# Performance work log

Hardware: AMD Instinct MI355X
Metric: run time of the kernel (lower is better)

## Reference

```python
import jax, jax.numpy as jnp
import numpy as np
import math

B, S, D = 2, 2048, 512
H = 8
DK = D // H  # 64


def setup_inputs() -> dict:
    key = jax.random.key(0)
    ks = jax.random.split(key, 9)
    inp = {
        "query": jax.random.normal(ks[0], (B, S, D), jnp.float32),
        "key": jax.random.normal(ks[1], (B, S, D), jnp.float32),
        "value": jax.random.normal(ks[2], (B, S, D), jnp.float32),
        "attn_weight": jax.random.normal(ks[3], (B, H, S, S), jnp.float32),
        "mask": jax.random.randint(ks[4], (B, S), 0, 2).astype(bool),
        # nn.Linear(d_model, d_model, bias=False) weights, applied as x @ W.T
        "Wq": jax.random.normal(ks[5], (D, D), jnp.float32) / math.sqrt(D),
        "Wk": jax.random.normal(ks[6], (D, D), jnp.float32) / math.sqrt(D),
        "Wv": jax.random.normal(ks[7], (D, D), jnp.float32) / math.sqrt(D),
        "Wo": jax.random.normal(ks[8], (D, D), jnp.float32) / math.sqrt(D),
    }
    return inp


def reference(query, key, value, attn_weight, mask, Wq, Wk, Wv, Wo):
    b, s, d = query.shape
    # project and split heads: [b, h, s, dk]
    def split_heads(x, W):
        return (x @ W.T).reshape(b, -1, H, DK).transpose(0, 2, 1, 3)

    q = split_heads(query, Wq)
    k = split_heads(key, Wk)
    v = split_heads(value, Wv)

    scores = jnp.einsum("bhqd,bhkd->bhqk", q, k) / math.sqrt(DK)
    # mask broadcast as [b,1,1,s]: True -> -inf over keys (applied before bias subtraction,
    # matching torch order; -inf - finite stays -inf)
    scores = jnp.where(mask[:, None, None, :], -jnp.inf, scores)
    scores = scores - attn_weight
    p_attn = jax.nn.softmax(scores, axis=-1)  # dropout p=0 (eval) -> identity
    x = jnp.einsum("bhqk,bhkd->bhqd", p_attn, v)
    x = x.transpose(0, 2, 1, 3).reshape(b, -1, H * DK)
    return x @ Wo.T
```

## Files before the change

### kernel.cpp

```cpp
#include <hip/hip_runtime.h>
#include <math.h>

typedef __bf16 bf16;
typedef __bf16 bf16x8 __attribute__((ext_vector_type(8)));
typedef float f32x4 __attribute__((ext_vector_type(4)));
typedef unsigned int u32;
typedef unsigned long long u64;

#define MFMA_BF16(a, b, c) __builtin_amdgcn_mfma_f32_16x16x32_bf16((a), (b), (c), 0, 0, 0)

static constexpr int kB = 2;
static constexpr int kS = 2048;
static constexpr int kD = 512;
static constexpr int kH = 8;
static constexpr int kDK = 64;
static constexpr int kTileBytes = 8192;
static constexpr int kBhBytes = 32 * kTileBytes;

__global__ void detect_mask_kernel(const unsigned char* __restrict__ m,
                                   u32* __restrict__ bm) {
  __shared__ int sh;
  const int tid = threadIdx.x;
  if (tid == 0) sh = 0;
  __syncthreads();
  int any = 0;
  for (int i = tid; i < kB * kS; i += 256)
    if ((i & 3) != 0 && m[i] != 0) any = 1;
  if (any) atomicOr(&sh, 1);
  __syncthreads();
  const bool as_bool = (sh != 0);
  for (int wi = tid; wi < kB * kS / 32; wi += 256) {
    u32 word = 0;
    const int base = wi * 32;
    for (int j = 0; j < 32; j++) {
      const bool mv = as_bool ? (m[base + j] != 0) : (((const int*)m)[base + j] != 0);
      word |= (mv ? 1u : 0u) << j;
    }
    bm[wi] = word;
  }
}

__device__ __forceinline__ void cvt16(const float* __restrict__ p, bf16x8& v0, bf16x8& v1) {
  const float4 fA = ((const float4*)p)[0];
  const float4 fB = ((const float4*)p)[1];
  const float4 fC = ((const float4*)p)[2];
  const float4 fD = ((const float4*)p)[3];
  v0[0] = (bf16)fA.x; v0[1] = (bf16)fA.y; v0[2] = (bf16)fA.z; v0[3] = (bf16)fA.w;
  v0[4] = (bf16)fB.x; v0[5] = (bf16)fB.y; v0[6] = (bf16)fB.z; v0[7] = (bf16)fB.w;
  v1[0] = (bf16)fC.x; v1[1] = (bf16)fC.y; v1[2] = (bf16)fC.z; v1[3] = (bf16)fC.w;
  v1[4] = (bf16)fD.x; v1[5] = (bf16)fD.y; v1[6] = (bf16)fD.z; v1[7] = (bf16)fD.w;
}

template <bool A_IS_F32, int MODE>
__device__ __forceinline__ void gemm_body(const void* __restrict__ Aptr,
                                          const float* __restrict__ Wptr,
                                          void* __restrict__ dst) {
  constexpr bool TRANS = (MODE != 2);
  __shared__ bf16 As[128][40];
  __shared__ bf16 Bs[128][40];

  const int tid = threadIdx.x;
  const int lane = tid & 63;
  const int w = tid >> 6;
  const int wr = w >> 1, wc = w & 1;
  const int l16 = lane & 15, g = lane >> 4;

  const int m_tile = blockIdx.x * 128;
  const int n_tile = blockIdx.y * 128;

  f32x4 acc[4][4] = {};

  const int sr = tid >> 1;
  const int sc = (tid & 1) * 16;

  for (int k0 = 0; k0 < kD; k0 += 32) {
    if constexpr (A_IS_F32) {
      const float* ap = (const float*)Aptr + (size_t)(m_tile + sr) * kD + k0 + sc;
      bf16x8 v0, v1;
      cvt16(ap, v0, v1);
      *(bf16x8*)&As[sr][sc] = v0;
      *(bf16x8*)&As[sr][sc + 8] = v1;
    } else {
      const bf16* ap = (const bf16*)Aptr + (size_t)(m_tile + sr) * kD + k0 + sc;
      *(bf16x8*)&As[sr][sc] = *(const bf16x8*)ap;
      *(bf16x8*)&As[sr][sc + 8] = *(const bf16x8*)(ap + 8);
    }
    {
      const float* bp = Wptr + (size_t)(n_tile + sr) * kD + k0 + sc;
      bf16x8 v0, v1;
      cvt16(bp, v0, v1);
      *(bf16x8*)&Bs[sr][sc] = v0;
      *(bf16x8*)&Bs[sr][sc + 8] = v1;
    }
    __syncthreads();

    bf16x8 a[4], bfr[4];
    #pragma unroll
    for (int i = 0; i < 4; i++)
      a[i] = *(const bf16x8*)&As[wr * 64 + i * 16 + l16][g * 8];
    #pragma unroll
    for (int i = 0; i < 4; i++)
      bfr[i] = *(const bf16x8*)&Bs[wc * 64 + i * 16 + l16][g * 8];
    #pragma unroll
    for (int mi = 0; mi < 4; mi++)
      #pragma unroll
      for (int ni = 0; ni < 4; ni++) {
        if constexpr (TRANS)
          acc[mi][ni] = MFMA_BF16(bfr[ni], a[mi], acc[mi][ni]);
        else
          acc[mi][ni] = MFMA_BF16(a[mi], bfr[ni], acc[mi][ni]);
      }
    __syncthreads();
  }

  #pragma unroll
  for (int mi = 0; mi < 4; mi++) {
    #pragma unroll
    for (int ni = 0; ni < 4; ni++) {
      const f32x4 v = acc[mi][ni];
      if constexpr (TRANS) {
        const int gm = m_tile + wr * 64 + mi * 16 + l16;
        const int gn0 = n_tile + wc * 64 + ni * 16 + g * 4;
        if constexpr (MODE == 3) {
          *(float4*)&((float*)dst)[(size_t)gm * kD + gn0] =
              (float4){v[0], v[1], v[2], v[3]};
        } else {
          const int bi = gm >> 11;
          const int s = gm & (kS - 1);
          const int h = gn0 >> 6;
          const int dk0 = gn0 & (kDK - 1);
          union { bf16 hh[4]; u64 u; } pk;
          pk.hh[0] = (bf16)v[0]; pk.hh[1] = (bf16)v[1];
          pk.hh[2] = (bf16)v[2]; pk.hh[3] = (bf16)v[3];
          if constexpr (MODE == 0) {
            *(u64*)&((bf16*)dst)[(((size_t)bi * kH + h) * kS + s) * kDK + dk0] = pk.u;
          } else {
            char* base = (char*)dst + (size_t)(bi * kH + h) * kBhBytes + (s >> 6) * kTileBytes;
            *(u64*)(base + (s & 63) * 128 + ((dk0 * 2) ^ ((s & 7) << 4))) = pk.u;
          }
        }
      } else {
        const int gm0 = m_tile + wr * 64 + mi * 16 + g * 4;
        const int gn = n_tile + wc * 64 + ni * 16 + l16;
        const int bi = gm0 >> 11;
        const int s0 = gm0 & (kS - 1);
        const int h = gn >> 6;
        const int dk = gn & (kDK - 1);
        union { bf16 hh[4]; u64 u; } pk;
        pk.hh[0] = (bf16)v[0]; pk.hh[1] = (bf16)v[1];
        pk.hh[2] = (bf16)v[2]; pk.hh[3] = (bf16)v[3];
        char* base = (char*)dst + (size_t)(bi * kH + h) * kBhBytes + (s0 >> 6) * kTileBytes;
        *(u64*)(base + dk * 128 + (((s0 & 63) * 2) ^ ((dk & 7) << 4))) = pk.u;
      }
    }
  }
}

__global__ __launch_bounds__(256) void proj_kernel(
    const float* __restrict__ q, const float* __restrict__ k, const float* __restrict__ v,
    const float* __restrict__ Wq, const float* __restrict__ Wk, const float* __restrict__ Wv,
    bf16* __restrict__ qw, bf16* __restrict__ kw, bf16* __restrict__ vtw) {
  const int z = blockIdx.z;
  if (z == 0) gemm_body<true, 0>(q, Wq, qw);
  else if (z == 1) gemm_body<true, 1>(k, Wk, kw);
  else gemm_body<true, 2>(v, Wv, vtw);
}

__global__ __launch_bounds__(256) void out_kernel(const bf16* __restrict__ x,
                                                  const float* __restrict__ Wo,
                                                  float* __restrict__ out) {
  gemm_body<false, 3>(x, Wo, out);
}

__global__ __launch_bounds__(256, 2) void attn_kernel(
    const bf16* __restrict__ qw, const char* __restrict__ kw,
    const char* __restrict__ vt, const float* __restrict__ bias,
    const u32* __restrict__ bmask, bf16* __restrict__ xw) {
  __shared__ char KV[2][2][kTileBytes];
  __shared__ u32 Ps[4][16][36];
  __shared__ u32 mask_lds[64];

  const int tid = threadIdx.x;
  const int lane = tid & 63;
  const int w = tid >> 6;
  const int l16 = lane & 15, g = lane >> 4;

  const int bid = blockIdx.x;
  const int xcd = bid & 7;
  const int j = bid >> 3;
  const int bh = xcd * 2 + (j >> 5);
  const int qb = j & 31;
  const int b = bh >> 3;
  const int hh = bh & 7;
  const int qr0 = qb * 64 + w * 16;

  if (tid < 64) mask_lds[tid] = bmask[b * 64 + tid];
  __syncthreads();

  const bf16* qrow = qw + ((size_t)bh * kS + qr0 + l16) * kDK;
  const bf16x8 aq0 = *(const bf16x8*)(qrow + g * 8);
  const bf16x8 aq1 = *(const bf16x8*)(qrow + 32 + g * 8);

  const float* brow = bias + ((size_t)bh * kS + qr0 + l16) * kS;
  const char* ktile = kw + (size_t)bh * kBhBytes;
  const char* vtile = vt + (size_t)bh * kBhBytes;

  f32x4 o[4] = {};
  float m_run = -__builtin_inff();
  float l_run = 0.f;
  const int swz = (l16 & 7) << 4;

  auto dma_tile = [&](int tile, int nb) {
    const char* kg = ktile + (size_t)tile * kTileBytes + w * 2048 + lane * 16;
    __builtin_amdgcn_global_load_lds(
        (const __attribute__((address_space(1))) void*)kg,
        (__attribute__((address_space(3))) void*)&KV[nb][0][w * 2048], 16, 0, 0);
    __builtin_amdgcn_global_load_lds(
        (const __attribute__((address_space(1))) void*)(kg + 1024),
        (__attribute__((address_space(3))) void*)&KV[nb][0][w * 2048 + 1024], 16, 0, 0);
    const char* vg = vtile + (size_t)tile * kTileBytes + w * 2048 + lane * 16;
    __builtin_amdgcn_global_load_lds(
        (const __attribute__((address_space(1))) void*)vg,
        (__attribute__((address_space(3))) void*)&KV[nb][1][w * 2048], 16, 0, 0);
    __builtin_amdgcn_global_load_lds(
        (const __attribute__((address_space(1))) void*)(vg + 1024),
        (__attribute__((address_space(3))) void*)&KV[nb][1][w * 2048 + 1024], 16, 0, 0);
  };
  auto load_bias_asm = [&](f32x4 (&bv)[4], int tile) {
    const float* p0 = brow + tile * 64 + g * 4;
    asm volatile("global_load_dwordx4 %0, %1, off" : "=v"(bv[0]) : "v"(p0));
    asm volatile("global_load_dwordx4 %0, %1, off" : "=v"(bv[1]) : "v"(p0 + 16));
    asm volatile("global_load_dwordx4 %0, %1, off" : "=v"(bv[2]) : "v"(p0 + 32));
    asm volatile("global_load_dwordx4 %0, %1, off" : "=v"(bv[3]) : "v"(p0 + 48));
  };

  auto phase = [&](int t, f32x4 (&bc)[4], f32x4 (&bn)[4]) {
    const int cur = t & 1, nxt = cur ^ 1;
    const int tp = (t + 1) & 31;
    dma_tile(tp, nxt);
    load_bias_asm(bn, tp);

    const char* kb0 = &KV[cur][0][0];
    const char* vb0 = &KV[cur][1][0];
    bf16x8 kf[4][2];
    #pragma unroll
    for (int nf = 0; nf < 4; nf++) {
      const int r = nf * 16 + l16;
      #pragma unroll
      for (int h = 0; h < 2; h++)
        kf[nf][h] = *(const bf16x8*)(kb0 + r * 128 + ((g * 16 + h * 64) ^ swz));
    }
    bf16x8 vf[2][4];
    #pragma unroll
    for (int kb2 = 0; kb2 < 2; kb2++)
      #pragma unroll
      for (int ni = 0; ni < 4; ni++) {
        const int d = ni * 16 + l16;
        vf[kb2][ni] = *(const bf16x8*)(vb0 + d * 128 + ((kb2 * 64 + g * 16) ^ swz));
      }

    const u32 w0 = mask_lds[2 * t];
    const u32 w1 = mask_lds[2 * t + 1];

    f32x4 sf[4];
    __builtin_amdgcn_s_setprio(1);
    #pragma unroll
    for (int nf = 0; nf < 4; nf++) {
      f32x4 z = {};
      z = MFMA_BF16(kf[nf][0], aq0, z);
      z = MFMA_BF16(kf[nf][1], aq1, z);
      sf[nf] = z;
    }
    __builtin_amdgcn_s_setprio(0);

    asm volatile("s_waitcnt vmcnt(8)" ::: "memory");
    __builtin_amdgcn_sched_barrier(0);

    float p[4][4];
    float tmax = -__builtin_inff();
    #pragma unroll
    for (int nf = 0; nf < 4; nf++) {
      const u32 wsel = (nf < 2) ? w0 : w1;
      #pragma unroll
      for (int r = 0; r < 4; r++) {
        float sv = sf[nf][r] * 0.125f - bc[nf][r];
        const int bp = (nf & 1) * 16 + g * 4 + r;
        if ((wsel >> bp) & 1) sv = -__builtin_inff();
        p[nf][r] = sv;
        tmax = fmaxf(tmax, sv);
      }
    }
    tmax = fmaxf(tmax, __shfl_xor(tmax, 16, 64));
    tmax = fmaxf(tmax, __shfl_xor(tmax, 32, 64));

    const float mnew = fmaxf(m_run, tmax);
    const float scale = (m_run == -__builtin_inff()) ? 0.f : __expf(m_run - mnew);
    const float mexp = (mnew == -__builtin_inff()) ? 0.f : mnew;
    float psum = 0.f;
    #pragma unroll
    for (int nf = 0; nf < 4; nf++)
      #pragma unroll
      for (int r = 0; r < 4; r++) {
        const float pv = __expf(p[nf][r] - mexp);
        p[nf][r] = pv;
        psum += pv;
      }
    psum += __shfl_xor(psum, 16, 64);
    psum += __shfl_xor(psum, 32, 64);
    m_run = mnew;
    l_run = l_run * scale + psum;
    #pragma unroll
    for (int ni = 0; ni < 4; ni++) o[ni] *= scale;

    #pragma unroll
    for (int nf = 0; nf < 4; nf++) {
      union { bf16 h[2]; u32 u; } c0, c1;
      c0.h[0] = (bf16)p[nf][0]; c0.h[1] = (bf16)p[nf][1];
      c1.h[0] = (bf16)p[nf][2]; c1.h[1] = (bf16)p[nf][3];
      Ps[w][l16][nf * 8 + g * 2] = c0.u;
      Ps[w][l16][nf * 8 + g * 2 + 1] = c1.u;
    }
    asm volatile("s_waitcnt lgkmcnt(0)" ::: "memory");

    __builtin_amdgcn_s_setprio(1);
    #pragma unroll
    for (int kb2 = 0; kb2 < 2; kb2++) {
      const bf16x8 pb = *(const bf16x8*)&Ps[w][l16][kb2 * 16 + g * 4];
      #pragma unroll
      for (int ni = 0; ni < 4; ni++)
        o[ni] = MFMA_BF16(vf[kb2][ni], pb, o[ni]);
    }
    __builtin_amdgcn_s_setprio(0);

    asm volatile("s_waitcnt vmcnt(4)" ::: "memory");
    __builtin_amdgcn_s_barrier();
    __builtin_amdgcn_sched_barrier(0);
  };

  f32x4 bc[4], bn[4];
  dma_tile(0, 0);
  load_bias_asm(bc, 0);
  asm volatile("s_waitcnt vmcnt(4)" ::: "memory");
  __builtin_amdgcn_s_barrier();
  __builtin_amdgcn_sched_barrier(0);

  for (int t = 0; t < 32; t += 2) {
    phase(t, bc, bn);
    phase(t + 1, bn, bc);
  }

  const float inv = (l_run > 0.f) ? 1.f / l_run : 0.f;
  bf16* dstp = xw + ((size_t)b * kS + qr0 + l16) * kD + hh * kDK;
  #pragma unroll
  for (int ni = 0; ni < 4; ni++) {
    union { bf16 h[2]; u32 u; } c0, c1;
    c0.h[0] = (bf16)(o[ni][0] * inv); c0.h[1] = (bf16)(o[ni][1] * inv);
    c1.h[0] = (bf16)(o[ni][2] * inv); c1.h[1] = (bf16)(o[ni][3] * inv);
    *(u32*)&dstp[ni * 16 + g * 4] = c0.u;
    *(u32*)&dstp[ni * 16 + g * 4 + 2] = c1.u;
  }
}

extern "C" void kernel_launch(void* const* d_in, const int* in_sizes, int n_in,
                              void* d_out, int out_size, void* d_ws, size_t ws_size,
                              hipStream_t stream) {
  (void)in_sizes; (void)n_in; (void)out_size; (void)ws_size;
  const float* query = (const float*)d_in[0];
  const float* key_in = (const float*)d_in[1];
  const float* value = (const float*)d_in[2];
  const float* attnw = (const float*)d_in[3];
  const unsigned char* mask = (const unsigned char*)d_in[4];
  const float* Wq = (const float*)d_in[5];
  const float* Wk = (const float*)d_in[6];
  const float* Wv = (const float*)d_in[7];
  const float* Wo = (const float*)d_in[8];

  const size_t nqkv = (size_t)kB * kH * kS * kDK;
  size_t off = 0;
  auto alloc = [&](size_t bytes) {
    void* p = (char*)d_ws + off;
    off = (off + bytes + 255) & ~(size_t)255;
    return p;
  };
  u32* bm = (u32*)alloc(kB * kS / 32 * 4);
  bf16* q_ws = (bf16*)alloc(nqkv * 2);
  char* k_ws = (char*)alloc(nqkv * 2);
  char* vt_ws = (char*)alloc(nqkv * 2);
  bf16* x_ws = (bf16*)alloc((size_t)kB * kS * kD * 2);

  detect_mask_kernel<<<1, 256, 0, stream>>>(mask, bm);

  proj_kernel<<<dim3(32, 4, 3), dim3(256), 0, stream>>>(query, key_in, value, Wq, Wk, Wv,
                                                        q_ws, (bf16*)k_ws, (bf16*)vt_ws);
  attn_kernel<<<dim3(512), dim3(256), 0, stream>>>(q_ws, k_ws, vt_ws, attnw, bm, x_ws);
  out_kernel<<<dim3(32, 4), dim3(256), 0, stream>>>(x_ws, Wo, (float*)d_out);
}
```

Baseline: 141.7 us.

## Triple-buffer attention K/V tiles with two-ahead prefetch and widen GEMM K-step

The attention kernel moves from double to triple buffering of K/V tiles in LDS. It prefetches K/V and bias two tiles ahead and rotates four bias register sets, with the vmcnt waits retuned to match. This gives more time to hide global load latency, at the cost of more LDS, more registers and redundant reloads of the last tile. Separately, the projection and output GEMMs now step K by 64 instead of 32, which halves the number of barrier-separated iterations and doubles the MFMAs issued per LDS fill.

Result: slower. 168.1 us (+18.7%).

```diff
diff --git a/kernel.cpp b/kernel.cpp
--- a/kernel.cpp
+++ b/kernel.cpp
@@ -56,8 +56,8 @@
                                           const float* __restrict__ Wptr,
                                           void* __restrict__ dst) {
   constexpr bool TRANS = (MODE != 2);
-  __shared__ bf16 As[128][40];
-  __shared__ bf16 Bs[128][40];
+  __shared__ bf16 As[128][72];
+  __shared__ bf16 Bs[128][72];
 
   const int tid = threadIdx.x;
   const int lane = tid & 63;
@@ -71,44 +71,56 @@
   f32x4 acc[4][4] = {};
 
   const int sr = tid >> 1;
-  const int sc = (tid & 1) * 16;
-
-  for (int k0 = 0; k0 < kD; k0 += 32) {
+  const int sc = (tid & 1) * 32;
+
+  for (int k0 = 0; k0 < kD; k0 += 64) {
     if constexpr (A_IS_F32) {
       const float* ap = (const float*)Aptr + (size_t)(m_tile + sr) * kD + k0 + sc;
-      bf16x8 v0, v1;
+      bf16x8 v0, v1, v2, v3;
       cvt16(ap, v0, v1);
+      cvt16(ap + 16, v2, v3);
       *(bf16x8*)&As[sr][sc] = v0;
       *(bf16x8*)&As[sr][sc + 8] = v1;
+      *(bf16x8*)&As[sr][sc + 16] = v2;
+      *(bf16x8*)&As[sr][sc + 24] = v3;
     } else {
       const bf16* ap = (const bf16*)Aptr + (size_t)(m_tile + sr) * kD + k0 + sc;
       *(bf16x8*)&As[sr][sc] = *(const bf16x8*)ap;
       *(bf16x8*)&As[sr][sc + 8] = *(const bf16x8*)(ap + 8);
+      *(bf16x8*)&As[sr][sc + 16] = *(const bf16x8*)(ap + 16);
+      *(bf16x8*)&As[sr][sc + 24] = *(const bf16x8*)(ap + 24);
     }
     {
       const float* bp = Wptr + (size_t)(n_tile + sr) * kD + k0 + sc;
-      bf16x8 v0, v1;
+      bf16x8 v0, v1, v2, v3;
       cvt16(bp, v0, v1);
+      cvt16(bp + 16, v2, v3);
       *(bf16x8*)&Bs[sr][sc] = v0;
       *(bf16x8*)&Bs[sr][sc + 8] = v1;
+      *(bf16x8*)&Bs[sr][sc + 16] = v2;
+      *(bf16x8*)&Bs[sr][sc + 24] = v3;
     }
     __syncthreads();
 
-    bf16x8 a[4], bfr[4];
+    bf16x8 a[4][2], bfr[4][2];
     #pragma unroll
     for (int i = 0; i < 4; i++)
-      a[i] = *(const bf16x8*)&As[wr * 64 + i * 16 + l16][g * 8];
-    #pragma unroll
-    for (int i = 0; i < 4; i++)
-      bfr[i] = *(const bf16x8*)&Bs[wc * 64 + i * 16 + l16][g * 8];
+      #pragma unroll
+      for (int h = 0; h < 2; h++) {
+        a[i][h] = *(const bf16x8*)&As[wr * 64 + i * 16 + l16][h * 32 + g * 8];
+        bfr[i][h] = *(const bf16x8*)&Bs[wc * 64 + i * 16 + l16][h * 32 + g * 8];
+      }
     #pragma unroll
     for (int mi = 0; mi < 4; mi++)
       #pragma unroll
       for (int ni = 0; ni < 4; ni++) {
-        if constexpr (TRANS)
-          acc[mi][ni] = MFMA_BF16(bfr[ni], a[mi], acc[mi][ni]);
-        else
-          acc[mi][ni] = MFMA_BF16(a[mi], bfr[ni], acc[mi][ni]);
+        if constexpr (TRANS) {
+          acc[mi][ni] = MFMA_BF16(bfr[ni][0], a[mi][0], acc[mi][ni]);
+          acc[mi][ni] = MFMA_BF16(bfr[ni][1], a[mi][1], acc[mi][ni]);
+        } else {
+          acc[mi][ni] = MFMA_BF16(a[mi][0], bfr[ni][0], acc[mi][ni]);
+          acc[mi][ni] = MFMA_BF16(a[mi][1], bfr[ni][1], acc[mi][ni]);
+        }
       }
     __syncthreads();
   }
@@ -176,7 +188,7 @@
     const bf16* __restrict__ qw, const char* __restrict__ kw,
     const char* __restrict__ vt, const float* __restrict__ bias,
     const u32* __restrict__ bmask, bf16* __restrict__ xw) {
-  __shared__ char KV[2][2][kTileBytes];
+  __shared__ char KV[3][2][kTileBytes];
   __shared__ u32 Ps[4][16][36];
   __shared__ u32 mask_lds[64];
 
@@ -234,14 +246,15 @@
     asm volatile("global_load_dwordx4 %0, %1, off" : "=v"(bv[3]) : "v"(p0 + 48));
   };
 
-  auto phase = [&](int t, f32x4 (&bc)[4], f32x4 (&bn)[4]) {
-    const int cur = t & 1, nxt = cur ^ 1;
-    const int tp = (t + 1) & 31;
-    dma_tile(tp, nxt);
-    load_bias_asm(bn, tp);
-
-    const char* kb0 = &KV[cur][0][0];
-    const char* vb0 = &KV[cur][1][0];
+  auto phase = [&](int t, f32x4 (&bc)[4], f32x4 (&bp2)[4]) {
+    const int c = t % 3;
+    const int c2 = (t + 2) % 3;
+    const int tp = (t + 2 > 31) ? 31 : t + 2;
+    dma_tile(tp, c2);
+    load_bias_asm(bp2, tp);
+
+    const char* kb0 = &KV[c][0][0];
+    const char* vb0 = &KV[c][1][0];
     bf16x8 kf[4][2];
     #pragma unroll
     for (int nf = 0; nf < 4; nf++) {
@@ -273,7 +286,7 @@
     }
     __builtin_amdgcn_s_setprio(0);
 
-    asm volatile("s_waitcnt vmcnt(8)" ::: "memory");
+    asm volatile("s_waitcnt vmcnt(16)" ::: "memory");
     __builtin_amdgcn_sched_barrier(0);
 
     float p[4][4];
@@ -332,21 +345,25 @@
     }
     __builtin_amdgcn_s_setprio(0);
 
-    asm volatile("s_waitcnt vmcnt(4)" ::: "memory");
+    asm volatile("s_waitcnt vmcnt(12)" ::: "memory");
     __builtin_amdgcn_s_barrier();
     __builtin_amdgcn_sched_barrier(0);
   };
 
-  f32x4 bc[4], bn[4];
+  f32x4 bA[4], bB[4], bC[4], bD[4];
   dma_tile(0, 0);
-  load_bias_asm(bc, 0);
-  asm volatile("s_waitcnt vmcnt(4)" ::: "memory");
+  load_bias_asm(bA, 0);
+  dma_tile(1, 1);
+  load_bias_asm(bB, 1);
+  asm volatile("s_waitcnt vmcnt(12)" ::: "memory");
   __builtin_amdgcn_s_barrier();
   __builtin_amdgcn_sched_barrier(0);
 
-  for (int t = 0; t < 32; t += 2) {
-    phase(t, bc, bn);
-    phase(t + 1, bn, bc);
+  for (int t = 0; t < 32; t += 4) {
+    phase(t, bA, bC);
+    phase(t + 1, bB, bD);
+    phase(t + 2, bC, bA);
+    phase(t + 3, bD, bB);
   }
 
   const float inv = (l_run > 0.f) ? 1.f / l_run : 0.f;
```

## Process 128-key blocks per attention pipeline phase instead of 64

Applied to the files above, without the earlier changes.

The flash-attention loop now handles two 64-key K/V tiles per phase: it loads 128 bias columns, computes 8 score fragments, and runs one online-softmax update per 128 keys. The number of phases, barriers and max/sum rescales is halved. In exchange it doubles LDS for the K/V double buffer, adds bias registers, and may lower occupancy. The final phase clamps its prefetch index to 15, so it issues a redundant load.

After: 137.1 us. 1.03x faster.

```diff
diff --git a/kernel.cpp b/kernel.cpp
--- a/kernel.cpp
+++ b/kernel.cpp
@@ -176,7 +176,7 @@
     const bf16* __restrict__ qw, const char* __restrict__ kw,
     const char* __restrict__ vt, const float* __restrict__ bias,
     const u32* __restrict__ bmask, bf16* __restrict__ xw) {
-  __shared__ char KV[2][2][kTileBytes];
+  __shared__ char KV[2][2][2 * kTileBytes];
   __shared__ u32 Ps[4][16][36];
   __shared__ u32 mask_lds[64];
 
@@ -210,77 +210,76 @@
   float l_run = 0.f;
   const int swz = (l16 & 7) << 4;
 
-  auto dma_tile = [&](int tile, int nb) {
-    const char* kg = ktile + (size_t)tile * kTileBytes + w * 2048 + lane * 16;
-    __builtin_amdgcn_global_load_lds(
-        (const __attribute__((address_space(1))) void*)kg,
-        (__attribute__((address_space(3))) void*)&KV[nb][0][w * 2048], 16, 0, 0);
-    __builtin_amdgcn_global_load_lds(
-        (const __attribute__((address_space(1))) void*)(kg + 1024),
-        (__attribute__((address_space(3))) void*)&KV[nb][0][w * 2048 + 1024], 16, 0, 0);
-    const char* vg = vtile + (size_t)tile * kTileBytes + w * 2048 + lane * 16;
-    __builtin_amdgcn_global_load_lds(
-        (const __attribute__((address_space(1))) void*)vg,
-        (__attribute__((address_space(3))) void*)&KV[nb][1][w * 2048], 16, 0, 0);
-    __builtin_amdgcn_global_load_lds(
-        (const __attribute__((address_space(1))) void*)(vg + 1024),
-        (__attribute__((address_space(3))) void*)&KV[nb][1][w * 2048 + 1024], 16, 0, 0);
+  auto dma_tile = [&](int t128, int nb) {
+    #pragma unroll
+    for (int s2 = 0; s2 < 2; s2++) {
+      const char* kg = ktile + ((size_t)t128 * 2 + s2) * kTileBytes + w * 2048 + lane * 16;
+      __builtin_amdgcn_global_load_lds(
+          (const __attribute__((address_space(1))) void*)kg,
+          (__attribute__((address_space(3))) void*)&KV[nb][0][s2 * kTileBytes + w * 2048], 16, 0, 0);
+      __builtin_amdgcn_global_load_lds(
+          (const __attribute__((address_space(1))) void*)(kg + 1024),
+          (__attribute__((address_space(3))) void*)&KV[nb][0][s2 * kTileBytes + w * 2048 + 1024], 16, 0, 0);
+      const char* vg = vtile + ((size_t)t128 * 2 + s2) * kTileBytes + w * 2048 + lane * 16;
+      __builtin_amdgcn_global_load_lds(
+          (const __attribute__((address_space(1))) void*)vg,
+          (__attribute__((address_space(3))) void*)&KV[nb][1][s2 * kTileBytes + w * 2048], 16, 0, 0);
+      __builtin_amdgcn_global_load_lds(
+          (const __attribute__((address_space(1))) void*)(vg + 1024),
+          (__attribute__((address_space(3))) void*)&KV[nb][1][s2 * kTileBytes + w * 2048 + 1024], 16, 0, 0);
+    }
   };
-  auto load_bias_asm = [&](f32x4 (&bv)[4], int tile) {
-    const float* p0 = brow + tile * 64 + g * 4;
+  auto load_bias8 = [&](f32x4 (&bv)[8], int t128) {
+    const float* p0 = brow + t128 * 128 + g * 4;
     asm volatile("global_load_dwordx4 %0, %1, off" : "=v"(bv[0]) : "v"(p0));
     asm volatile("global_load_dwordx4 %0, %1, off" : "=v"(bv[1]) : "v"(p0 + 16));
     asm volatile("global_load_dwordx4 %0, %1, off" : "=v"(bv[2]) : "v"(p0 + 32));
     asm volatile("global_load_dwordx4 %0, %1, off" : "=v"(bv[3]) : "v"(p0 + 48));
+    asm volatile("global_load_dwordx4 %0, %1, off" : "=v"(bv[4]) : "v"(p0 + 64));
+    asm volatile("global_load_dwordx4 %0, %1, off" : "=v"(bv[5]) : "v"(p0 + 80));
+    asm volatile("global_load_dwordx4 %0, %1, off" : "=v"(bv[6]) : "v"(p0 + 96));
+    asm volatile("global_load_dwordx4 %0, %1, off" : "=v"(bv[7]) : "v"(p0 + 112));
   };
 
-  auto phase = [&](int t, f32x4 (&bc)[4], f32x4 (&bn)[4]) {
+  auto phase = [&](int t, f32x4 (&bc)[8], f32x4 (&bn)[8]) {
     const int cur = t & 1, nxt = cur ^ 1;
-    const int tp = (t + 1) & 31;
+    const int tp = (t + 1 > 15) ? 15 : t + 1;
     dma_tile(tp, nxt);
-    load_bias_asm(bn, tp);
-
-    const char* kb0 = &KV[cur][0][0];
-    const char* vb0 = &KV[cur][1][0];
-    bf16x8 kf[4][2];
-    #pragma unroll
-    for (int nf = 0; nf < 4; nf++) {
-      const int r = nf * 16 + l16;
-      #pragma unroll
-      for (int h = 0; h < 2; h++)
-        kf[nf][h] = *(const bf16x8*)(kb0 + r * 128 + ((g * 16 + h * 64) ^ swz));
-    }
-    bf16x8 vf[2][4];
-    #pragma unroll
-    for (int kb2 = 0; kb2 < 2; kb2++)
-      #pragma unroll
-      for (int ni = 0; ni < 4; ni++) {
-        const int d = ni * 16 + l16;
-        vf[kb2][ni] = *(const bf16x8*)(vb0 + d * 128 + ((kb2 * 64 + g * 16) ^ swz));
-      }
-
-    const u32 w0 = mask_lds[2 * t];
-    const u32 w1 = mask_lds[2 * t + 1];
-
-    f32x4 sf[4];
-    __builtin_amdgcn_s_setprio(1);
-    #pragma unroll
-    for (int nf = 0; nf < 4; nf++) {
-      f32x4 z = {};
-      z = MFMA_BF16(kf[nf][0], aq0, z);
-      z = MFMA_BF16(kf[nf][1], aq1, z);
-      sf[nf] = z;
-    }
-    __builtin_amdgcn_s_setprio(0);
-
-    asm volatile("s_waitcnt vmcnt(8)" ::: "memory");
+    load_bias8(bn, tp);
+
+    f32x4 sf[8];
+    #pragma unroll
+    for (int hb = 0; hb < 2; hb++) {
+      const char* kb0 = &KV[cur][0][hb * kTileBytes];
+      bf16x8 kf[4][2];
+      #pragma unroll
+      for (int nf = 0; nf < 4; nf++) {
+        const int r = nf * 16 + l16;
+        #pragma unroll
+        for (int h = 0; h < 2; h++)
+          kf[nf][h] = *(const bf16x8*)(kb0 + r * 128 + ((g * 16 + h * 64) ^ swz));
+      }
+      __builtin_amdgcn_s_setprio(1);
+      #pragma unroll
+      for (int nf = 0; nf < 4; nf++) {
+        f32x4 z = {};
+        z = MFMA_BF16(kf[nf][0], aq0, z);
+        z = MFMA_BF16(kf[nf][1], aq1, z);
+        sf[hb * 4 + nf] = z;
+      }
+      __builtin_amdgcn_s_setprio(0);
+    }
+
+    asm volatile("s_waitcnt vmcnt(16)" ::: "memory");
     __builtin_amdgcn_sched_barrier(0);
 
-    float p[4][4];
+    const u32 wm0 = mask_lds[4 * t], wm1 = mask_lds[4 * t + 1];
+    const u32 wm2 = mask_lds[4 * t + 2], wm3 = mask_lds[4 * t + 3];
+    float p[8][4];
     float tmax = -__builtin_inff();
     #pragma unroll
-    for (int nf = 0; nf < 4; nf++) {
-      const u32 wsel = (nf < 2) ? w0 : w1;
+    for (int nf = 0; nf < 8; nf++) {
+      const u32 wsel = (nf < 2) ? wm0 : (nf < 4) ? wm1 : (nf < 6) ? wm2 : wm3;
       #pragma unroll
       for (int r = 0; r < 4; r++) {
         float sv = sf[nf][r] * 0.125f - bc[nf][r];
@@ -298,7 +297,7 @@
     const float mexp = (mnew == -__builtin_inff()) ? 0.f : mnew;
     float psum = 0.f;
     #pragma unroll
-    for (int nf = 0; nf < 4; nf++)
+    for (int nf = 0; nf < 8; nf++)
       #pragma unroll
       for (int r = 0; r < 4; r++) {
         const float pv = __expf(p[nf][r] - mexp);
@@ -313,38 +312,49 @@
     for (int ni = 0; ni < 4; ni++) o[ni] *= scale;
 
     #pragma unroll
-    for (int nf = 0; nf < 4; nf++) {
-      union { bf16 h[2]; u32 u; } c0, c1;
-      c0.h[0] = (bf16)p[nf][0]; c0.h[1] = (bf16)p[nf][1];
-      c1.h[0] = (bf16)p[nf][2]; c1.h[1] = (bf16)p[nf][3];
-      Ps[w][l16][nf * 8 + g * 2] = c0.u;
-      Ps[w][l16][nf * 8 + g * 2 + 1] = c1.u;
-    }
-    asm volatile("s_waitcnt lgkmcnt(0)" ::: "memory");
-
-    __builtin_amdgcn_s_setprio(1);
-    #pragma unroll
-    for (int kb2 = 0; kb2 < 2; kb2++) {
-      const bf16x8 pb = *(const bf16x8*)&Ps[w][l16][kb2 * 16 + g * 4];
-      #pragma unroll
-      for (int ni = 0; ni < 4; ni++)
-        o[ni] = MFMA_BF16(vf[kb2][ni], pb, o[ni]);
-    }
-    __builtin_amdgcn_s_setprio(0);
-
-    asm volatile("s_waitcnt vmcnt(4)" ::: "memory");
+    for (int hb = 0; hb < 2; hb++) {
+      #pragma unroll
+      for (int nf = 0; nf < 4; nf++) {
+        union { bf16 h2[2]; u32 u; } c0, c1;
+        c0.h2[0] = (bf16)p[hb * 4 + nf][0]; c0.h2[1] = (bf16)p[hb * 4 + nf][1];
+        c1.h2[0] = (bf16)p[hb * 4 + nf][2]; c1.h2[1] = (bf16)p[hb * 4 + nf][3];
+        Ps[w][l16][nf * 8 + g * 2] = c0.u;
+        Ps[w][l16][nf * 8 + g * 2 + 1] = c1.u;
+      }
+      asm volatile("s_waitcnt lgkmcnt(0)" ::: "memory");
+      const char* vb0 = &KV[cur][1][hb * kTileBytes];
+      bf16x8 vf[2][4];
+      #pragma unroll
+      for (int kb2 = 0; kb2 < 2; kb2++)
+        #pragma unroll
+        for (int ni = 0; ni < 4; ni++) {
+          const int d = ni * 16 + l16;
+          vf[kb2][ni] = *(const bf16x8*)(vb0 + d * 128 + ((kb2 * 64 + g * 16) ^ swz));
+        }
+      __builtin_amdgcn_s_setprio(1);
+      #pragma unroll
+      for (int kb2 = 0; kb2 < 2; kb2++) {
+        const bf16x8 pb = *(const bf16x8*)&Ps[w][l16][kb2 * 16 + g * 4];
+        #pragma unroll
+        for (int ni = 0; ni < 4; ni++)
+          o[ni] = MFMA_BF16(vf[kb2][ni], pb, o[ni]);
+      }
+      __builtin_amdgcn_s_setprio(0);
+    }
+
+    asm volatile("s_waitcnt vmcnt(8)" ::: "memory");
     __builtin_amdgcn_s_barrier();
     __builtin_amdgcn_sched_barrier(0);
   };
 
-  f32x4 bc[4], bn[4];
+  f32x4 bc[8], bn[8];
   dma_tile(0, 0);
-  load_bias_asm(bc, 0);
-  asm volatile("s_waitcnt vmcnt(4)" ::: "memory");
+  load_bias8(bc, 0);
+  asm volatile("s_waitcnt vmcnt(8)" ::: "memory");
   __builtin_amdgcn_s_barrier();
   __builtin_amdgcn_sched_barrier(0);
 
-  for (int t = 0; t < 32; t += 2) {
+  for (int t = 0; t < 16; t += 2) {
     phase(t, bc, bn);
     phase(t + 1, bn, bc);
   }
@@ -353,9 +363,9 @@
   bf16* dstp = xw + ((size_t)b * kS + qr0 + l16) * kD + hh * kDK;
   #pragma unroll
   for (int ni = 0; ni < 4; ni++) {
-    union { bf16 h[2]; u32 u; } c0, c1;
-    c0.h[0] = (bf16)(o[ni][0] * inv); c0.h[1] = (bf16)(o[ni][1] * inv);
-    c1.h[0] = (bf16)(o[ni][2] * inv); c1.h[1] = (bf16)(o[ni][3] * inv);
+    union { bf16 h2[2]; u32 u; } c0, c1;
+    c0.h2[0] = (bf16)(o[ni][0] * inv); c0.h2[1] = (bf16)(o[ni][1] * inv);
+    c1.h2[0] = (bf16)(o[ni][2] * inv); c1.h2[1] = (bf16)(o[ni][3] * inv);
     *(u32*)&dstp[ni * 16 + g * 4] = c0.u;
     *(u32*)&dstp[ni * 16 + g * 4 + 2] = c1.u;
   }
```

## Single-buffer V in LDS, load it in-phase, raise attention occupancy to four blocks

Applied to the files above, without the earlier changes.

Splits the combined K/V double buffer into a double-buffered K and a single-buffered V. The V tile for the current step is now fetched at the start of the same phase and waited on behind a new mid-phase barrier before the PV MFMAs. This cuts LDS use per block, and launch bounds go from 2 to 4 blocks per CU to raise occupancy and hide latency. The cost is an extra barrier per tile, V load latency exposed inside each phase, and a tighter register budget that could cause spills.

Measured after the change: 149.7 us. 5.7% more time.

```diff
diff --git a/kernel.cpp b/kernel.cpp
--- a/kernel.cpp
+++ b/kernel.cpp
@@ -172,11 +172,12 @@
   gemm_body<false, 3>(x, Wo, out);
 }
 
-__global__ __launch_bounds__(256, 2) void attn_kernel(
+__global__ __launch_bounds__(256, 4) void attn_kernel(
     const bf16* __restrict__ qw, const char* __restrict__ kw,
     const char* __restrict__ vt, const float* __restrict__ bias,
     const u32* __restrict__ bmask, bf16* __restrict__ xw) {
-  __shared__ char KV[2][2][kTileBytes];
+  __shared__ char Kb[2][kTileBytes];
+  __shared__ char Vb[kTileBytes];
   __shared__ u32 Ps[4][16][36];
   __shared__ u32 mask_lds[64];
 
@@ -210,21 +211,23 @@
   float l_run = 0.f;
   const int swz = (l16 & 7) << 4;
 
-  auto dma_tile = [&](int tile, int nb) {
+  auto dma_K = [&](int tile, int nb) {
     const char* kg = ktile + (size_t)tile * kTileBytes + w * 2048 + lane * 16;
     __builtin_amdgcn_global_load_lds(
         (const __attribute__((address_space(1))) void*)kg,
-        (__attribute__((address_space(3))) void*)&KV[nb][0][w * 2048], 16, 0, 0);
+        (__attribute__((address_space(3))) void*)&Kb[nb][w * 2048], 16, 0, 0);
     __builtin_amdgcn_global_load_lds(
         (const __attribute__((address_space(1))) void*)(kg + 1024),
-        (__attribute__((address_space(3))) void*)&KV[nb][0][w * 2048 + 1024], 16, 0, 0);
+        (__attribute__((address_space(3))) void*)&Kb[nb][w * 2048 + 1024], 16, 0, 0);
+  };
+  auto dma_V = [&](int tile) {
     const char* vg = vtile + (size_t)tile * kTileBytes + w * 2048 + lane * 16;
     __builtin_amdgcn_global_load_lds(
         (const __attribute__((address_space(1))) void*)vg,
-        (__attribute__((address_space(3))) void*)&KV[nb][1][w * 2048], 16, 0, 0);
+        (__attribute__((address_space(3))) void*)&Vb[w * 2048], 16, 0, 0);
     __builtin_amdgcn_global_load_lds(
         (const __attribute__((address_space(1))) void*)(vg + 1024),
-        (__attribute__((address_space(3))) void*)&KV[nb][1][w * 2048 + 1024], 16, 0, 0);
+        (__attribute__((address_space(3))) void*)&Vb[w * 2048 + 1024], 16, 0, 0);
   };
   auto load_bias_asm = [&](f32x4 (&bv)[4], int tile) {
     const float* p0 = brow + tile * 64 + g * 4;
@@ -235,13 +238,13 @@
   };
 
   auto phase = [&](int t, f32x4 (&bc)[4], f32x4 (&bn)[4]) {
-    const int cur = t & 1, nxt = cur ^ 1;
-    const int tp = (t + 1) & 31;
-    dma_tile(tp, nxt);
-    load_bias_asm(bn, tp);
-
-    const char* kb0 = &KV[cur][0][0];
-    const char* vb0 = &KV[cur][1][0];
+    const int cur = t & 1;
+    const int tp = (t + 1 > 31) ? 31 : t + 1;
+    dma_V(t);
+    dma_K(tp, tp & 1);
+    load_bias_asm(bn, (t + 1) & 31);
+
+    const char* kb0 = &Kb[cur][0];
     bf16x8 kf[4][2];
     #pragma unroll
     for (int nf = 0; nf < 4; nf++) {
@@ -250,18 +253,6 @@
       for (int h = 0; h < 2; h++)
         kf[nf][h] = *(const bf16x8*)(kb0 + r * 128 + ((g * 16 + h * 64) ^ swz));
     }
-    bf16x8 vf[2][4];
-    #pragma unroll
-    for (int kb2 = 0; kb2 < 2; kb2++)
-      #pragma unroll
-      for (int ni = 0; ni < 4; ni++) {
-        const int d = ni * 16 + l16;
-        vf[kb2][ni] = *(const bf16x8*)(vb0 + d * 128 + ((kb2 * 64 + g * 16) ^ swz));
-      }
-
-    const u32 w0 = mask_lds[2 * t];
-    const u32 w1 = mask_lds[2 * t + 1];
-
     f32x4 sf[4];
     __builtin_amdgcn_s_setprio(1);
     #pragma unroll
@@ -276,6 +267,8 @@
     asm volatile("s_waitcnt vmcnt(8)" ::: "memory");
     __builtin_amdgcn_sched_barrier(0);
 
+    const u32 w0 = mask_lds[2 * t];
+    const u32 w1 = mask_lds[2 * t + 1];
     float p[4][4];
     float tmax = -__builtin_inff();
     #pragma unroll
@@ -312,16 +305,28 @@
     #pragma unroll
     for (int ni = 0; ni < 4; ni++) o[ni] *= scale;
 
+    asm volatile("s_waitcnt vmcnt(6)" ::: "memory");
+    __builtin_amdgcn_s_barrier();
+    __builtin_amdgcn_sched_barrier(0);
+
     #pragma unroll
     for (int nf = 0; nf < 4; nf++) {
-      union { bf16 h[2]; u32 u; } c0, c1;
-      c0.h[0] = (bf16)p[nf][0]; c0.h[1] = (bf16)p[nf][1];
-      c1.h[0] = (bf16)p[nf][2]; c1.h[1] = (bf16)p[nf][3];
+      union { bf16 h2[2]; u32 u; } c0, c1;
+      c0.h2[0] = (bf16)p[nf][0]; c0.h2[1] = (bf16)p[nf][1];
+      c1.h2[0] = (bf16)p[nf][2]; c1.h2[1] = (bf16)p[nf][3];
       Ps[w][l16][nf * 8 + g * 2] = c0.u;
       Ps[w][l16][nf * 8 + g * 2 + 1] = c1.u;
     }
     asm volatile("s_waitcnt lgkmcnt(0)" ::: "memory");
 
+    bf16x8 vf[2][4];
+    #pragma unroll
+    for (int kb2 = 0; kb2 < 2; kb2++)
+      #pragma unroll
+      for (int ni = 0; ni < 4; ni++) {
+        const int d = ni * 16 + l16;
+        vf[kb2][ni] = *(const bf16x8*)(&Vb[0] + d * 128 + ((kb2 * 64 + g * 16) ^ swz));
+      }
     __builtin_amdgcn_s_setprio(1);
     #pragma unroll
     for (int kb2 = 0; kb2 < 2; kb2++) {
@@ -338,7 +343,7 @@
   };
 
   f32x4 bc[4], bn[4];
-  dma_tile(0, 0);
+  dma_K(0, 0);
   load_bias_asm(bc, 0);
   asm volatile("s_waitcnt vmcnt(4)" ::: "memory");
   __builtin_amdgcn_s_barrier();
@@ -353,9 +358,9 @@
   bf16* dstp = xw + ((size_t)b * kS + qr0 + l16) * kD + hh * kDK;
   #pragma unroll
   for (int ni = 0; ni < 4; ni++) {
-    union { bf16 h[2]; u32 u; } c0, c1;
-    c0.h[0] = (bf16)(o[ni][0] * inv); c0.h[1] = (bf16)(o[ni][1] * inv);
-    c1.h[0] = (bf16)(o[ni][2] * inv); c1.h[1] = (bf16)(o[ni][3] * inv);
+    union { bf16 h2[2]; u32 u; } c0, c1;
+    c0.h2[0] = (bf16)(o[ni][0] * inv); c0.h2[1] = (bf16)(o[ni][1] * inv);
+    c1.h2[0] = (bf16)(o[ni][2] * inv); c1.h2[1] = (bf16)(o[ni][3] * inv);
     *(u32*)&dstp[ni * 16 + g * 4] = c0.u;
     *(u32*)&dstp[ni * 16 + g * 4 + 2] = c1.u;
   }
```
